# Kernel optimization log

Measured on AMD Instinct MI355X. Metric: run time of the kernel, lower is better.

The kernel has to match this reference:

```python
import jax, jax.numpy as jnp
import numpy as np

H = 4      # hidden_size
L = 5      # num_layers
IN = 1     # input_size
B = 1024   # batch
T = 2048   # seq_len


def setup_inputs() -> dict:
    key = jax.random.key(0)
    ks = jax.random.split(key, 6)
    s = 1.0 / np.sqrt(H)  # PyTorch LSTM init: U(-1/sqrt(H), 1/sqrt(H))
    u = lambda k, shape: jax.random.uniform(k, shape, jnp.float32, -s, s)
    return {
        "x": jax.random.normal(ks[0], (B, T, IN), jnp.float32),
        "w_ih0": u(ks[1], (4 * H, IN)),          # layer 0 input weights
        "w_ih_rest": u(ks[2], (L - 1, 4 * H, H)),  # layers 1..L-1 input weights
        "w_hh": u(ks[3], (L, 4 * H, H)),
        "b_ih": u(ks[4], (L, 4 * H)),
        "b_hh": u(ks[5], (L, 4 * H)),
    }


def _lstm_layer(seq, w_ih, w_hh, b_ih, b_hh):
    # seq: [T, B, in] -> outputs [T, B, H], final hidden [B, H]
    # Precompute input contributions for all timesteps (one big GEMM).
    gx = jnp.einsum('tbi,gi->tbg', seq, w_ih) + b_ih + b_hh  # [T, B, 4H]
    h0 = jnp.zeros((seq.shape[1], H), seq.dtype)
    c0 = h0

    def step(carry, g_t):
        h, c = carry
        g = g_t + h @ w_hh.T                      # [B, 4H]
        i, f, gc, o = jnp.split(g, 4, axis=-1)    # PyTorch gate order i,f,g,o
        i = jax.nn.sigmoid(i)
        f = jax.nn.sigmoid(f)
        o = jax.nn.sigmoid(o)
        c = f * c + i * jnp.tanh(gc)
        h = o * jnp.tanh(c)
        return (h, c), h

    (hT, _), out = jax.lax.scan(step, (h0, c0), gx)
    return out, hT


def reference(x, w_ih0, w_ih_rest, w_hh, b_ih, b_hh):
    seq = jnp.transpose(x, (1, 0, 2))  # batch_first -> time-major [T, B, IN]
    out, hT = _lstm_layer(seq, w_ih0, w_hh[0], b_ih[0], b_hh[0])
    for l in range(L - 1):  # fixed small layer count; structural loop is fine
        out, hT = _lstm_layer(out, w_ih_rest[l], w_hh[l + 1], b_ih[l + 1], b_hh[l + 1])
    # final hidden state of the last (top) layer == rnn_hidden_states[-1]
    return hT  # [B, H]
```

## Files before the change

kernel.cpp:

```cpp
#include <hip/hip_runtime.h>
#include <stdint.h>


#define T_LEN   2048
#define NLAYER  5
#define CHUNK   32
#define NCHUNK  (T_LEN / CHUNK)
#define NPHASE  (NCHUNK + NLAYER - 1)
#define ROWSTR  33

template <int CTRL>
__device__ __forceinline__ float dppmov(float x) {
  int v = __builtin_amdgcn_mov_dpp(__float_as_int(x), CTRL, 0xF, 0xF, true);
  return __int_as_float(v);
}

template <bool PUSH>
__device__ __forceinline__ void lstm_step(
    float gxv, const float* whh, float k1, float k0,
    const float* wnx, float bnx,
    float& hr0, float& hr1, float& hr2, float& hr3, float& c,
    float* __restrict__ slot)
{
  const float LOG2E = 1.4426950408889634f;

  float t01 = fmaf(whh[0], hr0, gxv);
  t01 = fmaf(whh[1], hr1, t01);
  float t23 = whh[2] * hr2;
  t23 = fmaf(whh[3], hr3, t23);
  const float acc = t01 + t23;

  const float E = __builtin_amdgcn_exp2f(acc);
  const float A = 1.f + E;
  const float R = __builtin_amdgcn_rcpf(A);
  const float act = fmaf(k1, R, k0);

  const float iv = dppmov<0x00>(act);
  const float fv = dppmov<0x55>(act);
  const float gv = dppmov<0xAA>(act);
  const float ov = dppmov<0xFF>(act);
  const float ov2 = ov + ov;
  const float ovm = -ov;

  c = fmaf(fv, c, iv * gv);
  const float ct = c * (-2.0f * LOG2E);
  const float E2 = __builtin_amdgcn_exp2f(ct);
  const float A2 = 1.f + E2;
  const float R2 = __builtin_amdgcn_rcpf(A2);
  const float h  = fmaf(ov2, R2, ovm);

  hr0 = h;
  hr1 = dppmov<0x124>(h);
  hr2 = dppmov<0x128>(h);
  hr3 = dppmov<0x12C>(h);

  if (PUSH) {
    float g = fmaf(wnx[0], hr0, bnx);
    g = fmaf(wnx[1], hr1, g);
    float g2 = wnx[2] * hr2;
    g2 = fmaf(wnx[3], hr3, g2);
    *slot = g + g2;
  }
}

__global__ void __launch_bounds__(64 * NLAYER, 1) lstm_pipe(
    const float* __restrict__ x,
    const float* __restrict__ w_ih0,
    const float* __restrict__ w_ih_rest,
    const float* __restrict__ w_hh,
    const float* __restrict__ b_ih,
    const float* __restrict__ b_hh,
    float* __restrict__ out)
{
  const int tid  = threadIdx.x;
  const int l    = tid >> 6;
  const int lane = tid & 63;
  const int q    = lane & 15;
  const int el   = lane >> 4;
  const int e    = blockIdx.x * 4 + el;
  const int gt   = q & 3;
  const int j    = q >> 2;
  const int r    = gt * 4 + j;

  const float LOG2E = 1.4426950408889634f;
  const float s  = (gt == 2) ? (-2.0f * LOG2E) : (-LOG2E);
  const float k1 = (gt == 2) ? 2.0f : 1.0f;
  const float k0 = (gt == 2) ? -1.0f : 0.0f;

  float whh[4];
  #pragma unroll
  for (int m = 0; m < 4; ++m)
    whh[m] = w_hh[l * 64 + r * 4 + ((j - m) & 3)] * s;

  float wnx[4] = {0.f, 0.f, 0.f, 0.f};
  float bnx = 0.f;
  if (l < NLAYER - 1) {
    #pragma unroll
    for (int m = 0; m < 4; ++m)
      wnx[m] = w_ih_rest[l * 64 + r * 4 + ((j - m) & 3)] * s;
    bnx = (b_ih[(l + 1) * 16 + r] + b_hh[(l + 1) * 16 + r]) * s;
  }

  float wx = 0.f, bias0 = 0.f;
  if (l == 0) {
    wx = w_ih0[r] * s;
    bias0 = (b_ih[r] + b_hh[r]) * s;
  }

  float hr0 = 0.f, hr1 = 0.f, hr2 = 0.f, hr3 = 0.f;
  float c = 0.f;

  __shared__ float buf[NLAYER - 1][2][64][ROWSTR];

  float gx[CHUNK];
  float xcur[CHUNK];

  if (l == 0) {
    #pragma unroll
    for (int tc = 0; tc < CHUNK; ++tc) xcur[tc] = x[e * T_LEN + tc];
  }

  for (int p = 0; p < NPHASE; ++p) {
    const int n = p - l;
    if (n >= 0 && n < NCHUNK) {
      const int par = n & 1;

      if (l == 0) {
        #pragma unroll
        for (int tc = 0; tc < CHUNK; ++tc)
          gx[tc] = fmaf(wx, xcur[tc], bias0);
        if (n + 1 < NCHUNK) {
          #pragma unroll
          for (int tc = 0; tc < CHUNK; ++tc)
            xcur[tc] = x[e * T_LEN + (n + 1) * CHUNK + tc];
        }
      } else {
        const float* row = &buf[l - 1][par][lane][0];
        #pragma unroll
        for (int tc = 0; tc < CHUNK; ++tc) gx[tc] = row[tc];
      }

      __builtin_amdgcn_s_setprio(1);
      if (l < NLAYER - 1) {
        float* slot = &buf[l][par][lane][0];
        #pragma unroll
        for (int tc = 0; tc < CHUNK; ++tc)
          lstm_step<true>(gx[tc], whh, k1, k0, wnx, bnx,
                          hr0, hr1, hr2, hr3, c, slot + tc);
      } else {
        #pragma unroll
        for (int tc = 0; tc < CHUNK; ++tc)
          lstm_step<false>(gx[tc], whh, k1, k0, nullptr, 0.f,
                           hr0, hr1, hr2, hr3, c, nullptr);
      }
      __builtin_amdgcn_s_setprio(0);
    }
    __syncthreads();
  }

  if (l == NLAYER - 1 && gt == 0) out[e * 4 + j] = hr0;
}

extern "C" void kernel_launch(void* const* d_in, const int* in_sizes, int n_in,
                              void* d_out, int out_size, void* d_ws, size_t ws_size,
                              hipStream_t stream) {
  const float* x     = (const float*)d_in[0];
  const float* wih0  = (const float*)d_in[1];
  const float* wrest = (const float*)d_in[2];
  const float* whh   = (const float*)d_in[3];
  const float* bih   = (const float*)d_in[4];
  const float* bhh   = (const float*)d_in[5];
  float* out = (float*)d_out;

  dim3 grid(256);
  dim3 block(64 * NLAYER);
  lstm_pipe<<<grid, block, 0, stream>>>(x, wih0, wrest, whh, bih, bhh, out);
}
```

Before: 287.4 us.

## Fold the tanh(c) output into the next step's recurrent matvec to shorten the dependency chain

```diff
diff --git a/kernel.cpp b/kernel.cpp
--- a/kernel.cpp
+++ b/kernel.cpp
@@ -17,48 +17,50 @@
 
 template <bool PUSH>
 __device__ __forceinline__ void lstm_step(
-    float gxv, const float* whh, float k1, float k0,
+    float gxb, float k1, float k0,
+    const float* whh,
     const float* wnx, float bnx,
-    float& hr0, float& hr1, float& hr2, float& hr3, float& c,
+    float& R2, float& c, float a[4], float& b, float& h,
     float* __restrict__ slot)
 {
-  const float LOG2E = 1.4426950408889634f;
-
-  float t01 = fmaf(whh[0], hr0, gxv);
-  t01 = fmaf(whh[1], hr1, t01);
-  float t23 = whh[2] * hr2;
-  t23 = fmaf(whh[3], hr3, t23);
-  const float acc = t01 + t23;
-
+  const float r1 = dppmov<0x124>(R2);
+  const float r2 = dppmov<0x128>(R2);
+  const float r3 = dppmov<0x12C>(R2);
+  float u = fmaf(a[0], R2, gxb);
+  u = fmaf(a[1], r1, u);
+  float v = a[2] * r2;
+  v = fmaf(a[3], r3, v);
+  const float acc = u + v;
   const float E = __builtin_amdgcn_exp2f(acc);
   const float A = 1.f + E;
   const float R = __builtin_amdgcn_rcpf(A);
   const float act = fmaf(k1, R, k0);
-
   const float iv = dppmov<0x00>(act);
   const float fv = dppmov<0x55>(act);
   const float gv = dppmov<0xAA>(act);
   const float ov = dppmov<0xFF>(act);
-  const float ov2 = ov + ov;
-  const float ovm = -ov;
-
   c = fmaf(fv, c, iv * gv);
-  const float ct = c * (-2.0f * LOG2E);
-  const float E2 = __builtin_amdgcn_exp2f(ct);
+  const float o1 = dppmov<0x124>(ov);
+  const float o2 = dppmov<0x128>(ov);
+  const float o3 = dppmov<0x12C>(ov);
+  const float p0 = whh[0] * ov;
+  const float p1 = whh[1] * o1;
+  const float p2 = whh[2] * o2;
+  const float p3 = whh[3] * o3;
+  b = (p0 + p1) + (p2 + p3);
+  a[0] = p0 + p0; a[1] = p1 + p1; a[2] = p2 + p2; a[3] = p3 + p3;
+  const float E2 = __builtin_amdgcn_exp2f(c);
   const float A2 = 1.f + E2;
-  const float R2 = __builtin_amdgcn_rcpf(A2);
-  const float h  = fmaf(ov2, R2, ovm);
-
-  hr0 = h;
-  hr1 = dppmov<0x124>(h);
-  hr2 = dppmov<0x128>(h);
-  hr3 = dppmov<0x12C>(h);
-
+  R2 = __builtin_amdgcn_rcpf(A2);
+  h = fmaf(ov + ov, R2, -ov);
   if (PUSH) {
-    float g = fmaf(wnx[0], hr0, bnx);
-    g = fmaf(wnx[1], hr1, g);
-    float g2 = wnx[2] * hr2;
-    g2 = fmaf(wnx[3], hr3, g2);
+    const float h1 = dppmov<0x124>(h);
+    const float h2 = dppmov<0x128>(h);
+    const float h3 = dppmov<0x12C>(h);
+    float g = fmaf(wnx[0], h, bnx);
+    g = fmaf(wnx[1], h1, g);
+    float g2 = wnx[2] * h2;
+    g2 = fmaf(wnx[3], h3, g2);
     *slot = g + g2;
   }
 }
@@ -84,8 +86,8 @@
 
   const float LOG2E = 1.4426950408889634f;
   const float s  = (gt == 2) ? (-2.0f * LOG2E) : (-LOG2E);
-  const float k1 = (gt == 2) ? 2.0f : 1.0f;
-  const float k0 = (gt == 2) ? -1.0f : 0.0f;
+  const float k1 = (gt == 2) ? (-4.0f * LOG2E) : 1.0f;
+  const float k0 = (gt == 2) ? ( 2.0f * LOG2E) : 0.0f;
 
   float whh[4];
   #pragma unroll
@@ -107,8 +109,11 @@
     bias0 = (b_ih[r] + b_hh[r]) * s;
   }
 
-  float hr0 = 0.f, hr1 = 0.f, hr2 = 0.f, hr3 = 0.f;
-  float c = 0.f;
+  float R2 = 0.5f;
+  float c  = 0.f;
+  float a[4] = {0.f, 0.f, 0.f, 0.f};
+  float b  = 0.f;
+  float h  = 0.f;
 
   __shared__ float buf[NLAYER - 1][2][64][ROWSTR];
 
@@ -139,26 +144,31 @@
         #pragma unroll
         for (int tc = 0; tc < CHUNK; ++tc) gx[tc] = row[tc];
       }
+      float gxb = gx[0] - b;
 
       __builtin_amdgcn_s_setprio(1);
       if (l < NLAYER - 1) {
         float* slot = &buf[l][par][lane][0];
         #pragma unroll
-        for (int tc = 0; tc < CHUNK; ++tc)
-          lstm_step<true>(gx[tc], whh, k1, k0, wnx, bnx,
-                          hr0, hr1, hr2, hr3, c, slot + tc);
+        for (int tc = 0; tc < CHUNK; ++tc) {
+          lstm_step<true>(gxb, k1, k0, whh, wnx, bnx, R2, c, a, b, h,
+                          slot + tc);
+          if (tc < CHUNK - 1) gxb = gx[tc + 1] - b;
+        }
       } else {
         #pragma unroll
-        for (int tc = 0; tc < CHUNK; ++tc)
-          lstm_step<false>(gx[tc], whh, k1, k0, nullptr, 0.f,
-                           hr0, hr1, hr2, hr3, c, nullptr);
+        for (int tc = 0; tc < CHUNK; ++tc) {
+          lstm_step<false>(gxb, k1, k0, whh, nullptr, 0.f, R2, c, a, b, h,
+                           nullptr);
+          if (tc < CHUNK - 1) gxb = gx[tc + 1] - b;
+        }
       }
       __builtin_amdgcn_s_setprio(0);
     }
     __syncthreads();
   }
 
-  if (l == NLAYER - 1 && gt == 0) out[e * 4 + j] = hr0;
+  if (l == NLAYER - 1 && gt == 0) out[e * 4 + j] = h;
 }
 
 extern "C" void kernel_launch(void* const* d_in, const int* in_sizes, int n_in,
```

New measurement: 349.7 us. 21.7% more time.
